# Optimization experiments

Measured on AMD Instinct MI355X. Metric: run time of the kernel, lower is better.

## Reference

```python
import jax, jax.numpy as jnp
import numpy as np

DIL = 2      # dilation of deformable depthwise conv (padding == dilation -> same size)
EPS = 1e-5   # BatchNorm eps
B, C, O, G, H, W = 4, 256, 256, 64, 64, 64


def conv2d(x, w, padding, dilation=1):
    return jax.lax.conv_general_dilated(
        x, w, window_strides=(1, 1), padding=[(padding, padding)] * 2,
        rhs_dilation=(dilation, dilation),
        dimension_numbers=("NCHW", "OIHW", "NCHW"))


def bn_inf(x, gamma, beta, mean, var):
    scale = (gamma / jnp.sqrt(var + EPS))[None, :, None, None]
    return (x - mean[None, :, None, None]) * scale + beta[None, :, None, None]


def bilinear_gather(xt, ys, xs):
    # xt: [B,H,W,C]; ys, xs: [B,K,H,W] float sample coords. Zero padding outside.
    Bb, Hh, Ww, Cc = xt.shape
    y0 = jnp.floor(ys)
    x0 = jnp.floor(xs)
    wy = (ys - y0)[..., None]
    wx = (xs - x0)[..., None]
    bidx = jnp.arange(Bb)[:, None, None, None]

    def gather(yi, xi):
        valid = (yi >= 0) & (yi < Hh) & (xi >= 0) & (xi < Ww)
        yc = jnp.clip(yi, 0, Hh - 1).astype(jnp.int32)
        xc = jnp.clip(xi, 0, Ww - 1).astype(jnp.int32)
        val = xt[bidx, yc, xc]            # [B,K,H,W,C]
        return val * valid[..., None].astype(xt.dtype)

    v00 = gather(y0, x0)
    v01 = gather(y0, x0 + 1)
    v10 = gather(y0 + 1, x0)
    v11 = gather(y0 + 1, x0 + 1)
    return (v00 * (1 - wy) * (1 - wx) + v01 * (1 - wy) * wx
            + v10 * wy * (1 - wx) + v11 * wy * wx)


def setup_inputs() -> dict:
    key = jax.random.key(0)
    ks = jax.random.split(key, 12)
    inp = {
        "x": jax.random.normal(ks[0], (B, C, H, W), jnp.float32),
        "grad_feats": jax.random.normal(ks[1], (B, G, H, W), jnp.float32),
        # offset block: conv3x3(G->18) + BN + ReLU
        "off_w": jax.random.normal(ks[2], (18, G, 3, 3), jnp.float32) / np.sqrt(G * 9),
        "off_gamma": 1.0 + 0.1 * jax.random.normal(ks[3], (18,), jnp.float32),
        "off_beta": 0.1 * jax.random.normal(ks[4], (18,), jnp.float32),
        "off_mean": 0.1 * jax.random.normal(ks[5], (18,), jnp.float32),
        "off_var": jax.random.uniform(ks[6], (18,), jnp.float32, 0.5, 1.5),
        # deformable separable conv: depthwise 3x3 (per-channel) then pointwise 1x1, no bias
        "dw_w": jax.random.normal(ks[7], (C, 3, 3), jnp.float32) / 3.0,
        "pw_w": jax.random.normal(ks[8], (O, C), jnp.float32) / np.sqrt(C),
        # output BN
        "bn_gamma": 1.0 + 0.1 * jax.random.normal(ks[9], (O,), jnp.float32),
        "bn_beta": 0.1 * jax.random.normal(ks[10], (O,), jnp.float32),
        "bn_mean": 0.1 * jax.random.normal(ks[11], (O,), jnp.float32),
        "bn_var": jnp.ones((O,), jnp.float32),
    }
    return inp


def reference(x, grad_feats, off_w, off_gamma, off_beta, off_mean, off_var,
              dw_w, pw_w, bn_gamma, bn_beta, bn_mean, bn_var):
    Bb, Cc, Hh, Ww = x.shape
    # offset block: conv3x3 + BN + ReLU -> [B,18,H,W]
    off = jax.nn.relu(bn_inf(conv2d(grad_feats, off_w, 1),
                             off_gamma, off_beta, off_mean, off_var))
    off = off.reshape(Bb, 9, 2, Hh, Ww)
    dy, dx = off[:, :, 0], off[:, :, 1]                     # [B,9,H,W]
    # base kernel grid: padding == dilation so tap offsets are (kh-1)*DIL
    kk = (jnp.arange(3, dtype=jnp.float32) - 1.0) * DIL
    ky = jnp.repeat(kk, 3)                                   # [9] row offsets
    kx = jnp.tile(kk, 3)                                     # [9] col offsets
    gy = jnp.arange(Hh, dtype=jnp.float32)[None, None, :, None] + ky[None, :, None, None] + dy
    gx = jnp.arange(Ww, dtype=jnp.float32)[None, None, None, :] + kx[None, :, None, None] + dx
    samp = bilinear_gather(x.transpose(0, 2, 3, 1), gy, gx)  # [B,9,H,W,C]
    out = jnp.einsum("bkhwc,ck->bchw", samp, dw_w.reshape(Cc, 9))   # depthwise
    out = jnp.einsum("bchw,oc->bohw", out, pw_w)                    # pointwise 1x1
    out = jax.nn.relu(bn_inf(out, bn_gamma, bn_beta, bn_mean, bn_var))
    return out
```

## Files before the change

kernel.cpp:

```cpp
#include <hip/hip_runtime.h>
#include <stdint.h>

#define Bn 4
#define Cn 256
#define On 256
#define Gn 64
#define Hn 64
#define Wn 64
#define HWn 4096
#define EPSf 1e-5f

#define WS_XT    0u
#define WS_OFF   8388608u
#define WS_PWB   9568256u
#define WS_WT    9699328u

typedef __attribute__((ext_vector_type(8))) short short8;
typedef __attribute__((ext_vector_type(4))) float f4;

__device__ __forceinline__ unsigned int bfround(float f) {
    unsigned int u = __float_as_uint(f);
    u += 0x7FFFu + ((u >> 16) & 1u);
    return u >> 16;
}
__device__ __forceinline__ float blo(unsigned u) { return __uint_as_float(u << 16); }
__device__ __forceinline__ float bhi(unsigned u) { return __uint_as_float(u & 0xFFFF0000u); }

__global__ __launch_bounds__(256, 4) void k_pre(const float* __restrict__ x,
                                                const float* __restrict__ pw_w,
                                                const float* __restrict__ off_w,
                                                char* __restrict__ ws)
{
    __shared__ float smem[4160];
    int tid = threadIdx.x, bid = blockIdx.x;

    if (bid < 1024) {
        unsigned short* xt = (unsigned short*)(ws + WS_XT);
        int pt = bid & 63, ct = (bid >> 6) & 3, b = bid >> 8;
        int p0 = pt * 64, c0 = ct * 64;
        const f4* x4 = (const f4*)(x + (size_t)b * Cn * HWn);
        #pragma unroll
        for (int it = 0; it < 4; ++it) {
            int v = it * 256 + tid;
            int ci = v >> 4, pj = v & 15;
            f4 f = __builtin_nontemporal_load(&x4[(size_t)(c0 + ci) * 1024 + (p0 >> 2) + pj]);
            smem[ci * 65 + pj * 4 + 0] = f[0];
            smem[ci * 65 + pj * 4 + 1] = f[1];
            smem[ci * 65 + pj * 4 + 2] = f[2];
            smem[ci * 65 + pj * 4 + 3] = f[3];
        }
        __syncthreads();
        unsigned short* xtb = xt + (size_t)b * HWn * Cn;
        #pragma unroll
        for (int it = 0; it < 2; ++it) {
            int u = it * 256 + tid;
            int pi = u >> 3, cj = u & 7;
            float f[8];
            #pragma unroll
            for (int j = 0; j < 8; ++j)
                f[j] = smem[(cj * 8 + j) * 65 + pi];
            uint4 pk;
            pk.x = bfround(f[0]) | (bfround(f[1]) << 16);
            pk.y = bfround(f[2]) | (bfround(f[3]) << 16);
            pk.z = bfround(f[4]) | (bfround(f[5]) << 16);
            pk.w = bfround(f[6]) | (bfround(f[7]) << 16);
            *(uint4*)(xtb + (size_t)(p0 + pi) * Cn + c0 + cj * 8) = pk;
        }
        return;
    }
    if (bid < 1056) {
        unsigned short* pwb = (unsigned short*)(ws + WS_PWB);
        const float4* p4 = (const float4*)pw_w;
        uint2* o2 = (uint2*)pwb;
        int base = (bid - 1024) * 512;
        #pragma unroll
        for (int i = 0; i < 2; ++i) {
            int id2 = base + i * 256 + tid;
            float4 f = p4[id2];
            uint2 pk;
            pk.x = bfround(f.x) | (bfround(f.y) << 16);
            pk.y = bfround(f.z) | (bfround(f.w) << 16);
            o2[id2] = pk;
        }
        return;
    }
    {
        float* wT = (float*)(ws + WS_WT);
        for (int i = tid; i < 10368; i += 256) {
            int ch = i / 576;
            int rem = i - ch * 576;
            int g = rem / 9;
            int r9 = rem - g * 9;
            int ty = r9 / 3, tx = r9 - ty * 3;
            wT[(g * 3 + ty) * 54 + tx * 18 + ch] = off_w[i];
        }
    }
}

__global__ __launch_bounds__(256, 4) void k_off(const float* __restrict__ gf,
                                                const float* __restrict__ wT,
                                                const float* __restrict__ og,
                                                const float* __restrict__ obt,
                                                const float* __restrict__ om,
                                                const float* __restrict__ ov,
                                                float* __restrict__ off)
{
    __shared__ float sred[4 * 18 * 65];
    int tid = threadIdx.x;
    int h = blockIdx.x, b = blockIdx.y;
    int lane = tid & 63;
    int wvU = __builtin_amdgcn_readfirstlane(tid >> 6);

    float acc[18];
    #pragma unroll
    for (int ch = 0; ch < 18; ++ch) acc[ch] = 0.f;

    const float* gfb = gf + (size_t)b * Gn * HWn;
    for (int gi = 0; gi < 16; ++gi) {
        int g = wvU * 16 + gi;
        const float* gfg = gfb + (size_t)g * HWn;
        float rv[3], su[3], sd[3];
        #pragma unroll
        for (int r = 0; r < 3; ++r) {
            int y = h - 1 + r;
            rv[r] = ((unsigned)y < 64u) ? gfg[y * 64 + lane] : 0.f;
        }
        #pragma unroll
        for (int r = 0; r < 3; ++r) {
            float u = __shfl_up(rv[r], 1);   su[r] = (lane == 0)  ? 0.f : u;
            float d = __shfl_down(rv[r], 1); sd[r] = (lane == 63) ? 0.f : d;
        }
        #pragma unroll
        for (int ty = 0; ty < 3; ++ty) {
            const float* wrow = wT + (g * 3 + ty) * 54;
            #pragma unroll
            for (int ch = 0; ch < 18; ++ch)
                acc[ch] += wrow[ch] * su[ty] + wrow[18 + ch] * rv[ty] + wrow[36 + ch] * sd[ty];
        }
    }

    #pragma unroll
    for (int ch = 0; ch < 18; ++ch)
        sred[(wvU * 18 + ch) * 65 + lane] = acc[ch];
    __syncthreads();

    float* obp = off + (size_t)(b * HWn + h * 64) * 18;
    for (int i = tid; i < 1152; i += 256) {
        int w = i / 18, ch = i - w * 18;
        float v = sred[ch * 65 + w] + sred[(18 + ch) * 65 + w]
                + sred[(36 + ch) * 65 + w] + sred[(54 + ch) * 65 + w];
        float s = og[ch] * rsqrtf(ov[ch] + EPSf);
        v = (v - om[ch]) * s + obt[ch];
        obp[i] = v > 0.f ? v : 0.f;
    }
}

#define TLD 264
__global__ __launch_bounds__(512, 6) void k_fuse(float* __restrict__ out,
                                                 const float* __restrict__ dw_w,
                                                 const float* __restrict__ bg,
                                                 const float* __restrict__ bb,
                                                 const float* __restrict__ bm,
                                                 const float* __restrict__ bv,
                                                 const char* __restrict__ ws)
{
    const unsigned short* __restrict__ xt  = (const unsigned short*)(ws + WS_XT);
    const unsigned short* __restrict__ pwb = (const unsigned short*)(ws + WS_PWB);
    const float* __restrict__ off = (const float*)(ws + WS_OFF);
    __shared__ float smeta[288 * 8];
    __shared__ float sdw[9 * 256];
    __shared__ unsigned short tl[32 * TLD];

    int bid = blockIdx.x;
    int b = bid >> 7;
    int local = bid & 127;
    int h = local >> 1;
    int w0 = (local & 1) << 5;
    int tid = threadIdx.x;

    for (int i = tid; i < 2304; i += 512) {
        int k = i >> 8, c = i & 255;
        sdw[i] = dw_w[c * 9 + k];
    }

    if (tid < 288) {
        int k = tid >> 5, wl = tid & 31;
        int w = w0 + wl;
        int kyi = k / 3, kxi = k - kyi * 3;
        const float* op = off + ((size_t)(b * HWn + h * 64 + w)) * 18 + 2 * k;
        float dy = op[0], dx = op[1];
        float gy = (float)(h + (kyi - 1) * 2) + dy;
        float gx = (float)(w + (kxi - 1) * 2) + dx;
        float fy = floorf(gy), fx = floorf(gx);
        float wy = gy - fy, wx = gx - fx;
        int y0 = (int)fy, x0 = (int)fx;
        int y1 = y0 + 1, x1 = x0 + 1;
        float m00 = ((unsigned)y0 < 64u && (unsigned)x0 < 64u) ? 1.f : 0.f;
        float m01 = ((unsigned)y0 < 64u && (unsigned)x1 < 64u) ? 1.f : 0.f;
        float m10 = ((unsigned)y1 < 64u && (unsigned)x0 < 64u) ? 1.f : 0.f;
        float m11 = ((unsigned)y1 < 64u && (unsigned)x1 < 64u) ? 1.f : 0.f;
        int y0c = min(max(y0, 0), 63), y1c = min(max(y1, 0), 63);
        int x0c = min(max(x0, 0), 63), x1c = min(max(x1, 0), 63);
        float4 mw;
        mw.x = (1.f - wy) * (1.f - wx) * m00;
        mw.y = (1.f - wy) * wx * m01;
        mw.z = wy * (1.f - wx) * m10;
        mw.w = wy * wx * m11;
        float4 mo;
        mo.x = __int_as_float((y0c * 64 + x0c) << 9);
        mo.y = __int_as_float((y0c * 64 + x1c) << 9);
        mo.z = __int_as_float((y1c * 64 + x0c) << 9);
        mo.w = __int_as_float((y1c * 64 + x1c) << 9);
        float4* s4w = (float4*)smeta;
        s4w[(k * 32 + wl) * 2] = mw;
        s4w[(k * 32 + wl) * 2 + 1] = mo;
    }
    __syncthreads();

    int lane = tid & 63, wave = tid >> 6;
    int half = lane >> 5, c8 = lane & 31;
    int c0 = c8 * 8;

    const char* xb = (const char*)(xt + (size_t)b * HWn * Cn);
    int laneByte = c8 * 16;
    const float4* s4 = (const float4*)smeta;
    #pragma unroll
    for (int iter = 0; iter < 2; ++iter) {
        int wl = iter * 16 + wave * 2 + half;
        float acc[8];
        #pragma unroll
        for (int j = 0; j < 8; ++j) acc[j] = 0.f;
        #pragma unroll 1
        for (int k = 0; k < 9; ++k) {
            float4 mw = s4[(k * 32 + wl) * 2];
            float4 mo = s4[(k * 32 + wl) * 2 + 1];
            float4 d0 = *(const float4*)(&sdw[k * 256 + c0]);
            float4 d1 = *(const float4*)(&sdw[k * 256 + c0 + 4]);
            uint4 qA = *(const uint4*)(xb + __float_as_int(mo.x) + laneByte);
            uint4 qB = *(const uint4*)(xb + __float_as_int(mo.y) + laneByte);
            uint4 qC = *(const uint4*)(xb + __float_as_int(mo.z) + laneByte);
            uint4 qD = *(const uint4*)(xb + __float_as_int(mo.w) + laneByte);
            const unsigned* uA = (const unsigned*)&qA;
            const unsigned* uB = (const unsigned*)&qB;
            const unsigned* uC = (const unsigned*)&qC;
            const unsigned* uD = (const unsigned*)&qD;
            const float* dk0 = (const float*)&d0;
            const float* dk1 = (const float*)&d1;
            #pragma unroll
            for (int j = 0; j < 4; ++j) {
                const float* dkj = (j < 2) ? dk0 : dk1;
                int jj = (j & 1) * 2;
                float sl = mw.x * blo(uA[j]) + mw.y * blo(uB[j]) + mw.z * blo(uC[j]) + mw.w * blo(uD[j]);
                float sh = mw.x * bhi(uA[j]) + mw.y * bhi(uB[j]) + mw.z * bhi(uC[j]) + mw.w * bhi(uD[j]);
                acc[2 * j]     += sl * dkj[jj];
                acc[2 * j + 1] += sh * dkj[jj + 1];
            }
        }
        uint4 pk;
        pk.x = bfround(acc[0]) | (bfround(acc[1]) << 16);
        pk.y = bfround(acc[2]) | (bfround(acc[3]) << 16);
        pk.z = bfround(acc[4]) | (bfround(acc[5]) << 16);
        pk.w = bfround(acc[6]) | (bfround(acc[7]) << 16);
        *(uint4*)(&tl[wl * TLD + c0]) = pk;
    }
    __syncthreads();

    int m0 = wave * 32;
    int row = lane & 15, quad = lane >> 4;
    f4 acc[2][2];
    #pragma unroll
    for (int i = 0; i < 2; ++i)
        #pragma unroll
        for (int j = 0; j < 2; ++j)
            acc[i][j] = (f4){0.f, 0.f, 0.f, 0.f};

    #pragma unroll 2
    for (int kq = 0; kq < 8; ++kq) {
        int kk = kq * 32 + quad * 8;
        short8 a[2], bf[2];
        #pragma unroll
        for (int mt = 0; mt < 2; ++mt)
            a[mt] = *(const short8*)(pwb + (size_t)(m0 + mt * 16 + row) * Cn + kk);
        #pragma unroll
        for (int nt = 0; nt < 2; ++nt)
            bf[nt] = *(const short8*)(&tl[(nt * 16 + row) * TLD + kk]);
        #pragma unroll
        for (int mt = 0; mt < 2; ++mt)
            #pragma unroll
            for (int nt = 0; nt < 2; ++nt)
                acc[mt][nt] = __builtin_amdgcn_mfma_f32_16x16x32_bf16(a[mt], bf[nt], acc[mt][nt], 0, 0, 0);
    }

    float* obp = out + (size_t)b * On * HWn + h * 64 + w0;
    #pragma unroll
    for (int mt = 0; mt < 2; ++mt) {
        #pragma unroll
        for (int r = 0; r < 4; ++r) {
            int o = m0 + mt * 16 + quad * 4 + r;
            float s = bg[o] * rsqrtf(bv[o] + EPSf);
            float sh = bb[o] - bm[o] * s;
            #pragma unroll
            for (int nt = 0; nt < 2; ++nt) {
                float v = acc[mt][nt][r] * s + sh;
                v = v > 0.f ? v : 0.f;
                __builtin_nontemporal_store(v, &obp[(size_t)o * HWn + nt * 16 + row]);
            }
        }
    }
}

extern "C" void kernel_launch(void* const* d_in, const int* in_sizes, int n_in,
                              void* d_out, int out_size, void* d_ws, size_t ws_size,
                              hipStream_t stream)
{
    const float* x     = (const float*)d_in[0];
    const float* gf    = (const float*)d_in[1];
    const float* off_w = (const float*)d_in[2];
    const float* og    = (const float*)d_in[3];
    const float* ob    = (const float*)d_in[4];
    const float* om    = (const float*)d_in[5];
    const float* ov    = (const float*)d_in[6];
    const float* dw_w  = (const float*)d_in[7];
    const float* pw_w  = (const float*)d_in[8];
    const float* bg    = (const float*)d_in[9];
    const float* bb    = (const float*)d_in[10];
    const float* bm    = (const float*)d_in[11];
    const float* bv    = (const float*)d_in[12];
    float* out = (float*)d_out;
    char* ws = (char*)d_ws;

    hipLaunchKernelGGL(k_pre, dim3(1057), dim3(256), 0, stream, x, pw_w, off_w, ws);
    hipLaunchKernelGGL(k_off, dim3(Hn, Bn), dim3(256), 0, stream,
                       gf, (const float*)(ws + WS_WT), og, ob, om, ov,
                       (float*)(ws + WS_OFF));
    hipLaunchKernelGGL(k_fuse, dim3(512), dim3(512), 0, stream,
                       out, dw_w, bg, bb, bm, bv, ws);
}
```

Measured before the change: 153.0 us.

## Merge offset conv into prep kernel and remap fuse blocks for XCD locality

Folds the offset-conv kernel into the preprocessing kernel as extra blocks, which removes one launch and the separate weight-transpose pass. The offset blocks now read off_w directly with strided uniform loads instead of reading the transposed copy. k_fuse block indices are remapped so that blocks landing on the same XCD share a batch and a contiguous run of rows, which should improve L2 reuse of the gathered input. The fuse kernel's occupancy hint drops from 6 to 4 blocks per CU, trading occupancy for register headroom. The offset blocks may also run slower because their weight loads are now strided.

```diff
diff --git a/kernel.cpp b/kernel.cpp
--- a/kernel.cpp
+++ b/kernel.cpp
@@ -13,7 +13,6 @@
 #define WS_XT    0u
 #define WS_OFF   8388608u
 #define WS_PWB   9568256u
-#define WS_WT    9699328u
 
 typedef __attribute__((ext_vector_type(8))) short short8;
 typedef __attribute__((ext_vector_type(4))) float f4;
@@ -26,12 +25,17 @@
 __device__ __forceinline__ float blo(unsigned u) { return __uint_as_float(u << 16); }
 __device__ __forceinline__ float bhi(unsigned u) { return __uint_as_float(u & 0xFFFF0000u); }
 
-__global__ __launch_bounds__(256, 4) void k_pre(const float* __restrict__ x,
-                                                const float* __restrict__ pw_w,
-                                                const float* __restrict__ off_w,
-                                                char* __restrict__ ws)
+__global__ __launch_bounds__(256, 4) void k_prep(const float* __restrict__ x,
+                                                 const float* __restrict__ pw_w,
+                                                 const float* __restrict__ off_w,
+                                                 const float* __restrict__ gf,
+                                                 const float* __restrict__ og,
+                                                 const float* __restrict__ obt,
+                                                 const float* __restrict__ om,
+                                                 const float* __restrict__ ov,
+                                                 char* __restrict__ ws)
 {
-    __shared__ float smem[4160];
+    __shared__ float smem[4680];
     int tid = threadIdx.x, bid = blockIdx.x;
 
     if (bid < 1024) {
@@ -85,78 +89,61 @@
         return;
     }
     {
-        float* wT = (float*)(ws + WS_WT);
-        for (int i = tid; i < 10368; i += 256) {
-            int ch = i / 576;
-            int rem = i - ch * 576;
-            int g = rem / 9;
-            int r9 = rem - g * 9;
-            int ty = r9 / 3, tx = r9 - ty * 3;
-            wT[(g * 3 + ty) * 54 + tx * 18 + ch] = off_w[i];
+        float* off = (float*)(ws + WS_OFF);
+        int idx = bid - 1056;
+        int h = idx & 63, b = idx >> 6;
+        int lane = tid & 63;
+        int wvU = __builtin_amdgcn_readfirstlane(tid >> 6);
+
+        float acc[18];
+        #pragma unroll
+        for (int ch = 0; ch < 18; ++ch) acc[ch] = 0.f;
+
+        const float* gfb = gf + (size_t)b * Gn * HWn;
+        for (int gi = 0; gi < 16; ++gi) {
+            int g = wvU * 16 + gi;
+            const float* gfg = gfb + (size_t)g * HWn;
+            float rv[3], su[3], sd[3];
+            #pragma unroll
+            for (int r = 0; r < 3; ++r) {
+                int y = h - 1 + r;
+                rv[r] = ((unsigned)y < 64u) ? gfg[y * 64 + lane] : 0.f;
+            }
+            #pragma unroll
+            for (int r = 0; r < 3; ++r) {
+                float u = __shfl_up(rv[r], 1);   su[r] = (lane == 0)  ? 0.f : u;
+                float d = __shfl_down(rv[r], 1); sd[r] = (lane == 63) ? 0.f : d;
+            }
+            #pragma unroll
+            for (int ty = 0; ty < 3; ++ty) {
+                const float* wb = off_w + g * 9 + ty * 3;
+                #pragma unroll
+                for (int ch = 0; ch < 18; ++ch)
+                    acc[ch] += wb[ch * 576 + 0] * su[ty]
+                             + wb[ch * 576 + 1] * rv[ty]
+                             + wb[ch * 576 + 2] * sd[ty];
+            }
+        }
+
+        #pragma unroll
+        for (int ch = 0; ch < 18; ++ch)
+            smem[(wvU * 18 + ch) * 65 + lane] = acc[ch];
+        __syncthreads();
+
+        float* obp = off + (size_t)(b * HWn + h * 64) * 18;
+        for (int i = tid; i < 1152; i += 256) {
+            int w = i / 18, ch = i - w * 18;
+            float v = smem[ch * 65 + w] + smem[(18 + ch) * 65 + w]
+                    + smem[(36 + ch) * 65 + w] + smem[(54 + ch) * 65 + w];
+            float s = og[ch] * rsqrtf(ov[ch] + EPSf);
+            v = (v - om[ch]) * s + obt[ch];
+            obp[i] = v > 0.f ? v : 0.f;
         }
     }
 }
 
-__global__ __launch_bounds__(256, 4) void k_off(const float* __restrict__ gf,
-                                                const float* __restrict__ wT,
-                                                const float* __restrict__ og,
-                                                const float* __restrict__ obt,
-                                                const float* __restrict__ om,
-                                                const float* __restrict__ ov,
-                                                float* __restrict__ off)
-{
-    __shared__ float sred[4 * 18 * 65];
-    int tid = threadIdx.x;
-    int h = blockIdx.x, b = blockIdx.y;
-    int lane = tid & 63;
-    int wvU = __builtin_amdgcn_readfirstlane(tid >> 6);
-
-    float acc[18];
-    #pragma unroll
-    for (int ch = 0; ch < 18; ++ch) acc[ch] = 0.f;
-
-    const float* gfb = gf + (size_t)b * Gn * HWn;
-    for (int gi = 0; gi < 16; ++gi) {
-        int g = wvU * 16 + gi;
-        const float* gfg = gfb + (size_t)g * HWn;
-        float rv[3], su[3], sd[3];
-        #pragma unroll
-        for (int r = 0; r < 3; ++r) {
-            int y = h - 1 + r;
-            rv[r] = ((unsigned)y < 64u) ? gfg[y * 64 + lane] : 0.f;
-        }
-        #pragma unroll
-        for (int r = 0; r < 3; ++r) {
-            float u = __shfl_up(rv[r], 1);   su[r] = (lane == 0)  ? 0.f : u;
-            float d = __shfl_down(rv[r], 1); sd[r] = (lane == 63) ? 0.f : d;
-        }
-        #pragma unroll
-        for (int ty = 0; ty < 3; ++ty) {
-            const float* wrow = wT + (g * 3 + ty) * 54;
-            #pragma unroll
-            for (int ch = 0; ch < 18; ++ch)
-                acc[ch] += wrow[ch] * su[ty] + wrow[18 + ch] * rv[ty] + wrow[36 + ch] * sd[ty];
-        }
-    }
-
-    #pragma unroll
-    for (int ch = 0; ch < 18; ++ch)
-        sred[(wvU * 18 + ch) * 65 + lane] = acc[ch];
-    __syncthreads();
-
-    float* obp = off + (size_t)(b * HWn + h * 64) * 18;
-    for (int i = tid; i < 1152; i += 256) {
-        int w = i / 18, ch = i - w * 18;
-        float v = sred[ch * 65 + w] + sred[(18 + ch) * 65 + w]
-                + sred[(36 + ch) * 65 + w] + sred[(54 + ch) * 65 + w];
-        float s = og[ch] * rsqrtf(ov[ch] + EPSf);
-        v = (v - om[ch]) * s + obt[ch];
-        obp[i] = v > 0.f ? v : 0.f;
-    }
-}
-
 #define TLD 264
-__global__ __launch_bounds__(512, 6) void k_fuse(float* __restrict__ out,
+__global__ __launch_bounds__(512, 4) void k_fuse(float* __restrict__ out,
                                                  const float* __restrict__ dw_w,
                                                  const float* __restrict__ bg,
                                                  const float* __restrict__ bb,
@@ -172,10 +159,10 @@
     __shared__ unsigned short tl[32 * TLD];
 
     int bid = blockIdx.x;
-    int b = bid >> 7;
-    int local = bid & 127;
-    int h = local >> 1;
-    int w0 = (local & 1) << 5;
+    int xcd = bid & 7, slot = bid >> 3;
+    int b = xcd >> 1;
+    int h = ((xcd & 1) << 5) | (slot >> 1);
+    int w0 = (slot & 1) << 5;
     int tid = threadIdx.x;
 
     for (int i = tid; i < 2304; i += 512) {
@@ -329,10 +316,8 @@
     float* out = (float*)d_out;
     char* ws = (char*)d_ws;
 
-    hipLaunchKernelGGL(k_pre, dim3(1057), dim3(256), 0, stream, x, pw_w, off_w, ws);
-    hipLaunchKernelGGL(k_off, dim3(Hn, Bn), dim3(256), 0, stream,
-                       gf, (const float*)(ws + WS_WT), og, ob, om, ov,
-                       (float*)(ws + WS_OFF));
+    hipLaunchKernelGGL(k_prep, dim3(1312), dim3(256), 0, stream,
+                       x, pw_w, off_w, gf, og, ob, om, ov, ws);
     hipLaunchKernelGGL(k_fuse, dim3(512), dim3(512), 0, stream,
                        out, dw_w, bg, bb, bm, bv, ws);
 }
```

Result: faster. 140.1 us (-8.5%).
